# Performance work log

Hardware: AMD Instinct MI355X
Metric: run time of the kernel (lower is better)

## Reference

```python
import jax, jax.numpy as jnp
import numpy as np
import math

D_POLY = 2  # polynomial order d
N_NODES = 50000
IN_FEATS = 128
H_FEATS = 64
N_EDGES = 800000


def calc_thetas(d):
    # Beta-wavelet polynomial coefficients (ascending order), matching calculate_theta2
    thetas = []
    for i in range(d + 1):
        p = np.poly1d([1.0])
        for _ in range(i):
            p = p * np.poly1d([0.5, 0.0])      # (x/2)
        for _ in range(d - i):
            p = p * np.poly1d([-0.5, 1.0])     # (1 - x/2)
        beta = math.gamma(i + 1) * math.gamma(d + 1 - i) / math.gamma(d + 2)
        p = p / beta
        asc = p.coeffs[::-1]                   # ascending coefficients
        asc = np.concatenate([asc, np.zeros(d + 1 - len(asc))])
        thetas.append(asc.astype(np.float32))
    return thetas

THETAS = calc_thetas(D_POLY)


def setup_inputs() -> dict:
    key = jax.random.key(0)
    ks = jax.random.split(key, 7)
    features = jax.random.normal(ks[0], (N_NODES, IN_FEATS), dtype=jnp.float32)
    src = jax.random.randint(ks[1], (N_EDGES,), 0, N_NODES)
    dst = jax.random.randint(ks[2], (N_EDGES,), 0, N_NODES)
    s1 = 1.0 / math.sqrt(IN_FEATS)
    W1 = jax.random.uniform(ks[3], (H_FEATS, IN_FEATS), jnp.float32, -s1, s1)
    b1 = jnp.zeros((H_FEATS,), jnp.float32)
    s2 = 1.0 / math.sqrt(H_FEATS * (D_POLY + 1))
    W2 = jax.random.uniform(ks[4], (H_FEATS, H_FEATS * (D_POLY + 1)), jnp.float32, -s2, s2)
    b2 = jnp.zeros((H_FEATS,), jnp.float32)
    return {"features": features, "src": src, "dst": dst,
            "W1": W1, "b1": b1, "W2": W2, "b2": b2}


def reference(features, src, dst, W1, b1, W2, b2):
    N = features.shape[0]
    # linear1 + ReLU
    x = jax.nn.relu(features @ W1.T + b1)  # [N, H]
    # D^{-1/2} from in-degrees (clamped at 1)
    deg = jax.ops.segment_sum(jnp.ones_like(dst, dtype=x.dtype), dst, num_segments=N)
    D_invsqrt = jnp.clip(deg, 1.0, None) ** -0.5  # [N]
    D_invsqrt = D_invsqrt[:, None]

    def unn_laplacian(f):
        # f - D^{-1/2} A D^{-1/2} f   (aggregation onto destination nodes)
        agg = jax.ops.segment_sum((f * D_invsqrt)[src], dst, num_segments=N)
        return f - agg * D_invsqrt

    outs = []
    for theta in THETAS:
        f = x
        h = theta[0] * x
        for k in range(1, len(theta)):
            f = unn_laplacian(f)
            h = h + theta[k] * f
        outs.append(h)
    feats_final = jnp.concatenate(outs, axis=-1)  # [N, H*(d+1)]
    return feats_final @ W2.T + b2
```

## Files before the change

kernel.cpp:

```cpp
#include <hip/hip_runtime.h>

#define NN 50000
#define NE 800000
#define INF 128
#define HF 64
#define K2 192
#define MAXDEG 64

#if __has_builtin(__builtin_amdgcn_cvt_pk_fp8_f32) && __has_builtin(__builtin_amdgcn_cvt_pk_f32_fp8)
#define FP8_HW 1
#else
#include <hip/hip_fp8.h>
#endif

typedef __attribute__((ext_vector_type(8))) short short8;
typedef __attribute__((ext_vector_type(4))) float float4v;
typedef __attribute__((ext_vector_type(2))) float float2v;
typedef __attribute__((ext_vector_type(4))) unsigned short ushort4v;
typedef __attribute__((ext_vector_type(2))) unsigned int uint2v;

__device__ inline unsigned short f2bf(float x) {
    unsigned int u = __float_as_uint(x);
    u += 0x7FFFu + ((u >> 16) & 1u);
    return (unsigned short)(u >> 16);
}
__device__ inline float bflo(unsigned int p) { return __uint_as_float(p << 16); }
__device__ inline float bfhi(unsigned int p) { return __uint_as_float(p & 0xFFFF0000u); }


__device__ inline unsigned int fp8_pack4(float a, float b, float c, float d) {
#ifdef FP8_HW
    unsigned int w = (unsigned int)__builtin_amdgcn_cvt_pk_fp8_f32(a, b, 0, false);
    w = (unsigned int)__builtin_amdgcn_cvt_pk_fp8_f32(c, d, (int)w, true);
    return w;
#else
    __hip_fp8_e4m3 qa(a), qb(b), qc(c), qd(d);
    return (unsigned int)qa.__x | ((unsigned int)qb.__x << 8) |
           ((unsigned int)qc.__x << 16) | ((unsigned int)qd.__x << 24);
#endif
}
__device__ inline unsigned char fp8_1(float a) {
#ifdef FP8_HW
    return (unsigned char)((unsigned int)__builtin_amdgcn_cvt_pk_fp8_f32(a, 0.f, 0, false) & 0xFFu);
#else
    __hip_fp8_e4m3 q(a);
    return (unsigned char)q.__x;
#endif
}
__device__ inline float2v fp8_lo2(unsigned int d) {
#ifdef FP8_HW
    return __builtin_amdgcn_cvt_pk_f32_fp8((int)d, false);
#else
    __hip_fp8_e4m3 x; float2v r;
    x.__x = (unsigned char)(d & 0xFF);        r[0] = (float)x;
    x.__x = (unsigned char)((d >> 8) & 0xFF); r[1] = (float)x;
    return r;
#endif
}
__device__ inline float2v fp8_hi2(unsigned int d) {
#ifdef FP8_HW
    return __builtin_amdgcn_cvt_pk_f32_fp8((int)d, true);
#else
    __hip_fp8_e4m3 x; float2v r;
    x.__x = (unsigned char)((d >> 16) & 0xFF); r[0] = (float)x;
    x.__x = (unsigned char)((d >> 24) & 0xFF); r[1] = (float)x;
    return r;
#endif
}


__global__ __launch_bounds__(256) void fill_ell_part(const int* __restrict__ src,
                                                     const int* __restrict__ dst,
                                                     int* __restrict__ cnt,
                                                     unsigned short* __restrict__ ell) {
    int chunk = blockIdx.x >> 3;
    int p     = blockIdx.x & 7;
    int e0 = (chunk * 256 + (int)threadIdx.x) * 4;
    if (e0 >= NE) return;
    int4 d4 = *reinterpret_cast<const int4*>(dst + e0);
    int dd[4] = {d4.x, d4.y, d4.z, d4.w};
#pragma unroll
    for (int j = 0; j < 4; ++j) {
        int d = dd[j];
        if (d / 6250 == p) {
            int pos = atomicAdd(&cnt[d], 1);
            if (pos < MAXDEG) ell[d * MAXDEG + pos] = (unsigned short)src[e0 + j];
        }
    }
}


__global__ void pack_b(const float* __restrict__ W1, const float* __restrict__ W2,
                       unsigned short* __restrict__ Bp1, unsigned short* __restrict__ Bp2,
                       int* __restrict__ cnt,
                       unsigned int* __restrict__ hb0w, unsigned int* __restrict__ hb1w) {
    int gid = blockIdx.x * 256 + threadIdx.x;
    for (int z = gid; z < NN; z += 20480) cnt[z] = 0;
    if (gid < 16) {
        hb0w[(size_t)NN * 16 + gid] = 0;
        hb1w[(size_t)NN * 16 + gid] = 0;
    }
    if (gid >= 20480) return;
    if (gid < 8192) {
        int j  = gid & 7;
        int l  = (gid >> 3) & 63;
        int nt = (gid >> 9) & 3;
        int kc = gid >> 11;
        int n = nt * 16 + (l & 15);
        int k = kc * 32 + (l >> 4) * 8 + j;
        Bp1[gid] = f2bf(W1[n * INF + k]);
    } else {
        int g = gid - 8192;
        int j  = g & 7;
        int l  = (g >> 3) & 63;
        int nt = (g >> 9) & 3;
        int kc = g >> 11;
        int n = nt * 16 + (l & 15);
        int k = kc * 32 + (l >> 4) * 8 + j;
        const float* row = W2 + (size_t)n * K2;
        float v;
        if (k < 64) {
            v = 3.0f * row[k];
        } else if (k < 128) {
            int c = k - 64;
            v = -3.0f * row[c] + 3.0f * row[64 + c];
        } else {
            int c = k - 128;
            v = 0.75f * row[c] - 1.5f * row[64 + c] + 0.75f * row[128 + c];
        }
        Bp2[g] = f2bf(v);
    }
}


__global__ __launch_bounds__(256) void gemm1_mfma(const float* __restrict__ F,
                                                  const unsigned short* __restrict__ Bp,
                                                  const float* __restrict__ b1,
                                                  const int* __restrict__ cnt,
                                                  unsigned short* __restrict__ xb,
                                                  unsigned char* __restrict__ hb0) {
    int tid  = threadIdx.x;
    int lane = tid & 63;
    int wv   = tid >> 6;
    int m0   = blockIdx.x * 64 + wv * 16;
    if (m0 >= NN) return;
    int mrow = lane & 15;
    int q    = lane >> 4;

    float4v acc[4];
#pragma unroll
    for (int nt = 0; nt < 4; ++nt) acc[nt] = (float4v){0.f, 0.f, 0.f, 0.f};

    const float* arow = F + (size_t)(m0 + mrow) * INF + q * 8;
#pragma unroll
    for (int kc = 0; kc < INF / 32; ++kc) {
        const float* ap = arow + kc * 32;
        float4v a0 = *reinterpret_cast<const float4v*>(ap);
        float4v a1 = *reinterpret_cast<const float4v*>(ap + 4);
        short8 af;
        af[0] = (short)f2bf(a0[0]); af[1] = (short)f2bf(a0[1]);
        af[2] = (short)f2bf(a0[2]); af[3] = (short)f2bf(a0[3]);
        af[4] = (short)f2bf(a1[0]); af[5] = (short)f2bf(a1[1]);
        af[6] = (short)f2bf(a1[2]); af[7] = (short)f2bf(a1[3]);
#pragma unroll
        for (int nt = 0; nt < 4; ++nt) {
            short8 bf = *reinterpret_cast<const short8*>(Bp + (((kc * 4 + nt) * 64 + lane) << 3));
            acc[nt] = __builtin_amdgcn_mfma_f32_16x16x32_bf16(af, bf, acc[nt], 0, 0, 0);
        }
    }

    float dn[4];
#pragma unroll
    for (int r = 0; r < 4; ++r) {
        int c = cnt[m0 + q * 4 + r];
        c = c > MAXDEG ? MAXDEG : c;
        dn[r] = rsqrtf((float)(c < 1 ? 1 : c));
    }

#pragma unroll
    for (int nt = 0; nt < 4; ++nt) {
        int n = nt * 16 + mrow;
        float bv = b1[n];
#pragma unroll
        for (int r = 0; r < 4; ++r) {
            int node = m0 + q * 4 + r;
            float v = acc[nt][r] + bv;
            v = v > 0.0f ? v : 0.0f;
            xb [(size_t)node * HF + n] = f2bf(v);
            hb0[(size_t)node * HF + n] = fp8_1(v * dn[r]);
        }
    }
}


__device__ inline void gather_accum(const unsigned int* __restrict__ hbd,
                                    int s0, int s1, int s2, int s3,
                                    int deg, int base, int jj,
                                    float2v& e01, float2v& e23) {
    float2v A0 = {0.f, 0.f}, A1 = {0.f, 0.f};
    float2v B0 = {0.f, 0.f}, B1 = {0.f, 0.f};
    float2v C0 = {0.f, 0.f}, C1 = {0.f, 0.f};
    float2v D0 = {0.f, 0.f}, D1 = {0.f, 0.f};
    for (int k = 0; k < deg; k += 4) {
        int o = base + (k >> 2);
        int t0 = __shfl(s0, o), t1 = __shfl(s1, o);
        int t2 = __shfl(s2, o), t3 = __shfl(s3, o);
        unsigned int p0 = hbd[(size_t)t0 * 16 + jj];
        unsigned int p1 = hbd[(size_t)t1 * 16 + jj];
        unsigned int p2 = hbd[(size_t)t2 * 16 + jj];
        unsigned int p3 = hbd[(size_t)t3 * 16 + jj];
        A0 += fp8_lo2(p0); A1 += fp8_hi2(p0);
        B0 += fp8_lo2(p1); B1 += fp8_hi2(p1);
        C0 += fp8_lo2(p2); C1 += fp8_hi2(p2);
        D0 += fp8_lo2(p3); D1 += fp8_hi2(p3);
    }
    e01 = (A0 + B0) + (C0 + D0);
    e23 = (A1 + B1) + (C1 + D1);
}


__global__ __launch_bounds__(256) void gather_quad(const unsigned short* __restrict__ ell,
                                                   const int* __restrict__ cnt,
                                                   const unsigned short* __restrict__ fin,
                                                   const unsigned int* __restrict__ hb,
                                                   unsigned short* __restrict__ fout,
                                                   unsigned int* __restrict__ hout) {
    int lane  = threadIdx.x & 63;
    int wv    = threadIdx.x >> 6;
    int which = lane >> 4;
    int jj    = lane & 15;
    int n = blockIdx.x * 16 + wv * 4 + which;
    int deg = cnt[n];
    deg = deg > MAXDEG ? MAXDEG : deg;

    ushort4v ids = *reinterpret_cast<const ushort4v*>(ell + (size_t)n * MAXDEG + jj * 4);
    int slot = jj * 4;
    int s0 = (slot + 0 < deg) ? (int)ids[0] : NN;
    int s1 = (slot + 1 < deg) ? (int)ids[1] : NN;
    int s2 = (slot + 2 < deg) ? (int)ids[2] : NN;
    int s3 = (slot + 3 < deg) ? (int)ids[3] : NN;

    float2v e01, e23;
    gather_accum(hb, s0, s1, s2, s3, deg, which * 16, jj, e01, e23);

    float dn = rsqrtf((float)(deg < 1 ? 1 : deg));

    uint2v xv = ((const uint2v*)fin)[(size_t)n * 16 + jj];
    float f0 = bflo(xv[0]) - e01[0] * dn;
    float f1 = bfhi(xv[0]) - e01[1] * dn;
    float f2 = bflo(xv[1]) - e23[0] * dn;
    float f3 = bfhi(xv[1]) - e23[1] * dn;
    uint2v ov;
    ov[0] = (unsigned int)f2bf(f0) | ((unsigned int)f2bf(f1) << 16);
    ov[1] = (unsigned int)f2bf(f2) | ((unsigned int)f2bf(f3) << 16);
    ((uint2v*)fout)[(size_t)n * 16 + jj] = ov;
    hout[(size_t)n * 16 + jj] = fp8_pack4(f0 * dn, f1 * dn, f2 * dn, f3 * dn);
}


__global__ __launch_bounds__(256) void gather_gemm2(const unsigned short* __restrict__ ell,
                                                    const int* __restrict__ cnt,
                                                    const unsigned short* __restrict__ xb,
                                                    const unsigned short* __restrict__ f1b,
                                                    const unsigned int* __restrict__ hb1,
                                                    const unsigned short* __restrict__ Bp,
                                                    const float* __restrict__ b2,
                                                    float* __restrict__ out) {
    __shared__ __align__(16) unsigned int xl [16 * 68];
    __shared__ __align__(16) unsigned int f1l[16 * 68];
    __shared__ __align__(16) unsigned int f2l[16 * 68];
    int tid   = threadIdx.x;
    int lane  = tid & 63;
    int wv    = tid >> 6;
    int which = lane >> 4;
    int jj    = lane & 15;
    int row   = wv * 4 + which;
    int n     = blockIdx.x * 16 + row;

    int deg = cnt[n];
    deg = deg > MAXDEG ? MAXDEG : deg;
    ushort4v ids = *reinterpret_cast<const ushort4v*>(ell + (size_t)n * MAXDEG + jj * 4);
    int slot = jj * 4;
    int s0 = (slot + 0 < deg) ? (int)ids[0] : NN;
    int s1 = (slot + 1 < deg) ? (int)ids[1] : NN;
    int s2 = (slot + 2 < deg) ? (int)ids[2] : NN;
    int s3 = (slot + 3 < deg) ? (int)ids[3] : NN;

    float2v e01, e23;
    gather_accum(hb1, s0, s1, s2, s3, deg, which * 16, jj, e01, e23);

    float dn = rsqrtf((float)(deg < 1 ? 1 : deg));
    uint2v xv  = ((const uint2v*)f1b)[(size_t)n * 16 + jj];
    uint2v xbv = ((const uint2v*)xb )[(size_t)n * 16 + jj];
    float f0 = bflo(xv[0]) - e01[0] * dn;
    float f1 = bfhi(xv[0]) - e01[1] * dn;
    float f2 = bflo(xv[1]) - e23[0] * dn;
    float f3 = bfhi(xv[1]) - e23[1] * dn;

    int o = row * 68 + jj * 2;
    xl [o] = xbv[0]; xl [o + 1] = xbv[1];
    f1l[o] = xv[0];  f1l[o + 1] = xv[1];
    f2l[o]     = (unsigned int)f2bf(f0) | ((unsigned int)f2bf(f1) << 16);
    f2l[o + 1] = (unsigned int)f2bf(f2) | ((unsigned int)f2bf(f3) << 16);

    __syncthreads();

    int mrow = lane & 15;
    int qq   = lane >> 4;
    float4v acc = (float4v){0.f, 0.f, 0.f, 0.f};

#pragma unroll
    for (int kc = 0; kc < 6; ++kc) {
        const unsigned int* srcT = (kc < 2) ? xl : (kc < 4) ? f1l : f2l;
        int kk = kc & 1;
        short8 af = *reinterpret_cast<const short8*>(srcT + mrow * 68 + kk * 16 + qq * 4);
        short8 bf = *reinterpret_cast<const short8*>(Bp + (((kc * 4 + wv) * 64 + lane) << 3));
        acc = __builtin_amdgcn_mfma_f32_16x16x32_bf16(af, bf, acc, 0, 0, 0);
    }

    int n2 = wv * 16 + mrow;
    float bv = b2[n2];
    int nb = blockIdx.x * 16;
#pragma unroll
    for (int r = 0; r < 4; ++r) {
        int node = nb + qq * 4 + r;
        out[(size_t)node * HF + n2] = acc[r] + bv;
    }
}


extern "C" void kernel_launch(void* const* d_in, const int* in_sizes, int n_in,
                              void* d_out, int out_size, void* d_ws, size_t ws_size,
                              hipStream_t stream) {
    const float* features = (const float*)d_in[0];
    const int*   src      = (const int*)d_in[1];
    const int*   dst      = (const int*)d_in[2];
    const float* W1       = (const float*)d_in[3];
    const float* b1       = (const float*)d_in[4];
    const float* W2       = (const float*)d_in[5];
    const float* b2       = (const float*)d_in[6];
    float* out = (float*)d_out;

    unsigned short* xb  = (unsigned short*)d_ws;
    unsigned char*  hb0 = (unsigned char*)(xb + (size_t)NN * HF);
    unsigned short* f1b = (unsigned short*)(hb0 + (size_t)(NN + 1) * HF);
    unsigned char*  hb1 = (unsigned char*)(f1b + (size_t)NN * HF);
    unsigned short* Bp1 = (unsigned short*)(hb1 + (size_t)(NN + 1) * HF);
    unsigned short* Bp2 = Bp1 + 8192;
    unsigned short* ell = Bp2 + 12288;
    int*   cnt  = (int*)(ell + (size_t)NN * MAXDEG);

    pack_b<<<80, 256, 0, stream>>>(W1, W2, Bp1, Bp2, cnt,
                                   (unsigned int*)hb0, (unsigned int*)hb1);

    fill_ell_part<<<((NE + 1023) / 1024) * 8, 256, 0, stream>>>(src, dst, cnt, ell);

    gemm1_mfma<<<(NN + 63) / 64, 256, 0, stream>>>(features, Bp1, b1, cnt, xb, hb0);

    gather_quad<<<NN / 16, 256, 0, stream>>>(ell, cnt, xb, (const unsigned int*)hb0,
                                             f1b, (unsigned int*)hb1);

    gather_gemm2<<<NN / 16, 256, 0, stream>>>(ell, cnt, xb, f1b,
                                              (const unsigned int*)hb1, Bp2, b2, out);
}
```

Measured before the change: 158.5 us.

## Fuse all stages into one persistent kernel with grid-wide barriers

Replaces the five separate launches (weight packing, ELL fill, GEMM1, two gather stages) with a single persistent kernel of 1024 blocks. The blocks loop over virtual work items and synchronize between stages through an atomic-counter grid barrier. The counters and barrier word are zeroed with a memset before the launch. This removes per-launch overhead and inter-kernel gaps, but it depends on all 1024 blocks being co-resident, which launch_bounds(256,4) is meant to ensure. The barriers also serialize stages with spin-waiting, which can cost time when stages are unevenly loaded.

```diff
diff --git a/kernel.cpp b/kernel.cpp
--- a/kernel.cpp
+++ b/kernel.cpp
@@ -6,6 +6,10 @@
 #define HF 64
 #define K2 192
 #define MAXDEG 64
+#define GRID 1024
+#define ELLB (((NE + 1023) / 1024) * 8)
+#define G1B  ((NN + 63) / 64)
+#define GQB  (NN / 16)
 
 #if __has_builtin(__builtin_amdgcn_cvt_pk_fp8_f32) && __has_builtin(__builtin_amdgcn_cvt_pk_f32_fp8)
 #define FP8_HW 1
@@ -69,127 +73,14 @@
 }
 
 
-__global__ __launch_bounds__(256) void fill_ell_part(const int* __restrict__ src,
-                                                     const int* __restrict__ dst,
-                                                     int* __restrict__ cnt,
-                                                     unsigned short* __restrict__ ell) {
-    int chunk = blockIdx.x >> 3;
-    int p     = blockIdx.x & 7;
-    int e0 = (chunk * 256 + (int)threadIdx.x) * 4;
-    if (e0 >= NE) return;
-    int4 d4 = *reinterpret_cast<const int4*>(dst + e0);
-    int dd[4] = {d4.x, d4.y, d4.z, d4.w};
-#pragma unroll
-    for (int j = 0; j < 4; ++j) {
-        int d = dd[j];
-        if (d / 6250 == p) {
-            int pos = atomicAdd(&cnt[d], 1);
-            if (pos < MAXDEG) ell[d * MAXDEG + pos] = (unsigned short)src[e0 + j];
-        }
-    }
-}
-
-
-__global__ void pack_b(const float* __restrict__ W1, const float* __restrict__ W2,
-                       unsigned short* __restrict__ Bp1, unsigned short* __restrict__ Bp2,
-                       int* __restrict__ cnt,
-                       unsigned int* __restrict__ hb0w, unsigned int* __restrict__ hb1w) {
-    int gid = blockIdx.x * 256 + threadIdx.x;
-    for (int z = gid; z < NN; z += 20480) cnt[z] = 0;
-    if (gid < 16) {
-        hb0w[(size_t)NN * 16 + gid] = 0;
-        hb1w[(size_t)NN * 16 + gid] = 0;
-    }
-    if (gid >= 20480) return;
-    if (gid < 8192) {
-        int j  = gid & 7;
-        int l  = (gid >> 3) & 63;
-        int nt = (gid >> 9) & 3;
-        int kc = gid >> 11;
-        int n = nt * 16 + (l & 15);
-        int k = kc * 32 + (l >> 4) * 8 + j;
-        Bp1[gid] = f2bf(W1[n * INF + k]);
-    } else {
-        int g = gid - 8192;
-        int j  = g & 7;
-        int l  = (g >> 3) & 63;
-        int nt = (g >> 9) & 3;
-        int kc = g >> 11;
-        int n = nt * 16 + (l & 15);
-        int k = kc * 32 + (l >> 4) * 8 + j;
-        const float* row = W2 + (size_t)n * K2;
-        float v;
-        if (k < 64) {
-            v = 3.0f * row[k];
-        } else if (k < 128) {
-            int c = k - 64;
-            v = -3.0f * row[c] + 3.0f * row[64 + c];
-        } else {
-            int c = k - 128;
-            v = 0.75f * row[c] - 1.5f * row[64 + c] + 0.75f * row[128 + c];
-        }
-        Bp2[g] = f2bf(v);
-    }
-}
-
-
-__global__ __launch_bounds__(256) void gemm1_mfma(const float* __restrict__ F,
-                                                  const unsigned short* __restrict__ Bp,
-                                                  const float* __restrict__ b1,
-                                                  const int* __restrict__ cnt,
-                                                  unsigned short* __restrict__ xb,
-                                                  unsigned char* __restrict__ hb0) {
-    int tid  = threadIdx.x;
-    int lane = tid & 63;
-    int wv   = tid >> 6;
-    int m0   = blockIdx.x * 64 + wv * 16;
-    if (m0 >= NN) return;
-    int mrow = lane & 15;
-    int q    = lane >> 4;
-
-    float4v acc[4];
-#pragma unroll
-    for (int nt = 0; nt < 4; ++nt) acc[nt] = (float4v){0.f, 0.f, 0.f, 0.f};
-
-    const float* arow = F + (size_t)(m0 + mrow) * INF + q * 8;
-#pragma unroll
-    for (int kc = 0; kc < INF / 32; ++kc) {
-        const float* ap = arow + kc * 32;
-        float4v a0 = *reinterpret_cast<const float4v*>(ap);
-        float4v a1 = *reinterpret_cast<const float4v*>(ap + 4);
-        short8 af;
-        af[0] = (short)f2bf(a0[0]); af[1] = (short)f2bf(a0[1]);
-        af[2] = (short)f2bf(a0[2]); af[3] = (short)f2bf(a0[3]);
-        af[4] = (short)f2bf(a1[0]); af[5] = (short)f2bf(a1[1]);
-        af[6] = (short)f2bf(a1[2]); af[7] = (short)f2bf(a1[3]);
-#pragma unroll
-        for (int nt = 0; nt < 4; ++nt) {
-            short8 bf = *reinterpret_cast<const short8*>(Bp + (((kc * 4 + nt) * 64 + lane) << 3));
-            acc[nt] = __builtin_amdgcn_mfma_f32_16x16x32_bf16(af, bf, acc[nt], 0, 0, 0);
-        }
-    }
-
-    float dn[4];
-#pragma unroll
-    for (int r = 0; r < 4; ++r) {
-        int c = cnt[m0 + q * 4 + r];
-        c = c > MAXDEG ? MAXDEG : c;
-        dn[r] = rsqrtf((float)(c < 1 ? 1 : c));
-    }
-
-#pragma unroll
-    for (int nt = 0; nt < 4; ++nt) {
-        int n = nt * 16 + mrow;
-        float bv = b1[n];
-#pragma unroll
-        for (int r = 0; r < 4; ++r) {
-            int node = m0 + q * 4 + r;
-            float v = acc[nt][r] + bv;
-            v = v > 0.0f ? v : 0.0f;
-            xb [(size_t)node * HF + n] = f2bf(v);
-            hb0[(size_t)node * HF + n] = fp8_1(v * dn[r]);
-        }
-    }
+__device__ inline void gbar(unsigned int* bar, unsigned int target) {
+    __syncthreads();
+    if (threadIdx.x == 0) {
+        __hip_atomic_fetch_add(bar, 1u, __ATOMIC_ACQ_REL, __HIP_MEMORY_SCOPE_AGENT);
+        while (__hip_atomic_load(bar, __ATOMIC_ACQUIRE, __HIP_MEMORY_SCOPE_AGENT) < target)
+            __builtin_amdgcn_s_sleep(8);
+    }
+    __syncthreads();
 }
 
 
@@ -219,112 +110,217 @@
 }
 
 
-__global__ __launch_bounds__(256) void gather_quad(const unsigned short* __restrict__ ell,
-                                                   const int* __restrict__ cnt,
-                                                   const unsigned short* __restrict__ fin,
-                                                   const unsigned int* __restrict__ hb,
-                                                   unsigned short* __restrict__ fout,
-                                                   unsigned int* __restrict__ hout) {
-    int lane  = threadIdx.x & 63;
-    int wv    = threadIdx.x >> 6;
-    int which = lane >> 4;
-    int jj    = lane & 15;
-    int n = blockIdx.x * 16 + wv * 4 + which;
-    int deg = cnt[n];
-    deg = deg > MAXDEG ? MAXDEG : deg;
-
-    ushort4v ids = *reinterpret_cast<const ushort4v*>(ell + (size_t)n * MAXDEG + jj * 4);
-    int slot = jj * 4;
-    int s0 = (slot + 0 < deg) ? (int)ids[0] : NN;
-    int s1 = (slot + 1 < deg) ? (int)ids[1] : NN;
-    int s2 = (slot + 2 < deg) ? (int)ids[2] : NN;
-    int s3 = (slot + 3 < deg) ? (int)ids[3] : NN;
-
-    float2v e01, e23;
-    gather_accum(hb, s0, s1, s2, s3, deg, which * 16, jj, e01, e23);
-
-    float dn = rsqrtf((float)(deg < 1 ? 1 : deg));
-
-    uint2v xv = ((const uint2v*)fin)[(size_t)n * 16 + jj];
-    float f0 = bflo(xv[0]) - e01[0] * dn;
-    float f1 = bfhi(xv[0]) - e01[1] * dn;
-    float f2 = bflo(xv[1]) - e23[0] * dn;
-    float f3 = bfhi(xv[1]) - e23[1] * dn;
-    uint2v ov;
-    ov[0] = (unsigned int)f2bf(f0) | ((unsigned int)f2bf(f1) << 16);
-    ov[1] = (unsigned int)f2bf(f2) | ((unsigned int)f2bf(f3) << 16);
-    ((uint2v*)fout)[(size_t)n * 16 + jj] = ov;
-    hout[(size_t)n * 16 + jj] = fp8_pack4(f0 * dn, f1 * dn, f2 * dn, f3 * dn);
-}
-
-
-__global__ __launch_bounds__(256) void gather_gemm2(const unsigned short* __restrict__ ell,
-                                                    const int* __restrict__ cnt,
-                                                    const unsigned short* __restrict__ xb,
-                                                    const unsigned short* __restrict__ f1b,
-                                                    const unsigned int* __restrict__ hb1,
-                                                    const unsigned short* __restrict__ Bp,
-                                                    const float* __restrict__ b2,
-                                                    float* __restrict__ out) {
+__global__ __launch_bounds__(256, 4) void mega(
+        const float* __restrict__ F, const int* __restrict__ src,
+        const int* __restrict__ dst, const float* __restrict__ W1,
+        const float* __restrict__ b1, const float* __restrict__ W2,
+        const float* __restrict__ b2, float* __restrict__ out,
+        unsigned short* __restrict__ xb, unsigned char* __restrict__ hb0,
+        unsigned short* __restrict__ f1b, unsigned char* __restrict__ hb1,
+        unsigned short* __restrict__ Bp1, unsigned short* __restrict__ Bp2,
+        unsigned short* __restrict__ ell, int* __restrict__ cnt,
+        unsigned int* __restrict__ bar) {
     __shared__ __align__(16) unsigned int xl [16 * 68];
     __shared__ __align__(16) unsigned int f1l[16 * 68];
     __shared__ __align__(16) unsigned int f2l[16 * 68];
+
     int tid   = threadIdx.x;
     int lane  = tid & 63;
     int wv    = tid >> 6;
     int which = lane >> 4;
     int jj    = lane & 15;
-    int row   = wv * 4 + which;
-    int n     = blockIdx.x * 16 + row;
-
-    int deg = cnt[n];
-    deg = deg > MAXDEG ? MAXDEG : deg;
-    ushort4v ids = *reinterpret_cast<const ushort4v*>(ell + (size_t)n * MAXDEG + jj * 4);
-    int slot = jj * 4;
-    int s0 = (slot + 0 < deg) ? (int)ids[0] : NN;
-    int s1 = (slot + 1 < deg) ? (int)ids[1] : NN;
-    int s2 = (slot + 2 < deg) ? (int)ids[2] : NN;
-    int s3 = (slot + 3 < deg) ? (int)ids[3] : NN;
-
-    float2v e01, e23;
-    gather_accum(hb1, s0, s1, s2, s3, deg, which * 16, jj, e01, e23);
-
-    float dn = rsqrtf((float)(deg < 1 ? 1 : deg));
-    uint2v xv  = ((const uint2v*)f1b)[(size_t)n * 16 + jj];
-    uint2v xbv = ((const uint2v*)xb )[(size_t)n * 16 + jj];
-    float f0 = bflo(xv[0]) - e01[0] * dn;
-    float f1 = bfhi(xv[0]) - e01[1] * dn;
-    float f2 = bflo(xv[1]) - e23[0] * dn;
-    float f3 = bfhi(xv[1]) - e23[1] * dn;
-
-    int o = row * 68 + jj * 2;
-    xl [o] = xbv[0]; xl [o + 1] = xbv[1];
-    f1l[o] = xv[0];  f1l[o + 1] = xv[1];
-    f2l[o]     = (unsigned int)f2bf(f0) | ((unsigned int)f2bf(f1) << 16);
-    f2l[o + 1] = (unsigned int)f2bf(f2) | ((unsigned int)f2bf(f3) << 16);
-
-    __syncthreads();
-
-    int mrow = lane & 15;
-    int qq   = lane >> 4;
-    float4v acc = (float4v){0.f, 0.f, 0.f, 0.f};
-
-#pragma unroll
-    for (int kc = 0; kc < 6; ++kc) {
-        const unsigned int* srcT = (kc < 2) ? xl : (kc < 4) ? f1l : f2l;
-        int kk = kc & 1;
-        short8 af = *reinterpret_cast<const short8*>(srcT + mrow * 68 + kk * 16 + qq * 4);
-        short8 bf = *reinterpret_cast<const short8*>(Bp + (((kc * 4 + wv) * 64 + lane) << 3));
-        acc = __builtin_amdgcn_mfma_f32_16x16x32_bf16(af, bf, acc, 0, 0, 0);
-    }
-
-    int n2 = wv * 16 + mrow;
-    float bv = b2[n2];
-    int nb = blockIdx.x * 16;
-#pragma unroll
-    for (int r = 0; r < 4; ++r) {
-        int node = nb + qq * 4 + r;
-        out[(size_t)node * HF + n2] = acc[r] + bv;
+
+    {
+        int gid = blockIdx.x * 256 + tid;
+        if (gid < 16) {
+            ((unsigned int*)hb0)[(size_t)NN * 16 + gid] = 0;
+            ((unsigned int*)hb1)[(size_t)NN * 16 + gid] = 0;
+        }
+        if (gid < 8192) {
+            int j  = gid & 7;
+            int l  = (gid >> 3) & 63;
+            int nt = (gid >> 9) & 3;
+            int kc = gid >> 11;
+            int n = nt * 16 + (l & 15);
+            int k = kc * 32 + (l >> 4) * 8 + j;
+            Bp1[gid] = f2bf(W1[n * INF + k]);
+        } else if (gid < 20480) {
+            int g = gid - 8192;
+            int j  = g & 7;
+            int l  = (g >> 3) & 63;
+            int nt = (g >> 9) & 3;
+            int kc = g >> 11;
+            int n = nt * 16 + (l & 15);
+            int k = kc * 32 + (l >> 4) * 8 + j;
+            const float* row = W2 + (size_t)n * K2;
+            float v;
+            if (k < 64) {
+                v = 3.0f * row[k];
+            } else if (k < 128) {
+                int c = k - 64;
+                v = -3.0f * row[c] + 3.0f * row[64 + c];
+            } else {
+                int c = k - 128;
+                v = 0.75f * row[c] - 1.5f * row[64 + c] + 0.75f * row[128 + c];
+            }
+            Bp2[g] = f2bf(v);
+        }
+    }
+
+    for (int vb = blockIdx.x; vb < ELLB; vb += GRID) {
+        int chunk = vb >> 3;
+        int p     = vb & 7;
+        int e0 = (chunk * 256 + tid) * 4;
+        if (e0 >= NE) continue;
+        int4 d4 = *reinterpret_cast<const int4*>(dst + e0);
+        int dd[4] = {d4.x, d4.y, d4.z, d4.w};
+#pragma unroll
+        for (int j = 0; j < 4; ++j) {
+            int d = dd[j];
+            if (d / 6250 == p) {
+                int pos = atomicAdd(&cnt[d], 1);
+                if (pos < MAXDEG) ell[d * MAXDEG + pos] = (unsigned short)src[e0 + j];
+            }
+        }
+    }
+    gbar(bar, GRID);
+
+    for (int tb = blockIdx.x; tb < G1B; tb += GRID) {
+        int m0 = tb * 64 + wv * 16;
+        if (m0 >= NN) continue;
+        int mrow = lane & 15;
+        int q    = lane >> 4;
+
+        float4v acc[4];
+#pragma unroll
+        for (int nt = 0; nt < 4; ++nt) acc[nt] = (float4v){0.f, 0.f, 0.f, 0.f};
+
+        const float* arow = F + (size_t)(m0 + mrow) * INF + q * 8;
+#pragma unroll
+        for (int kc = 0; kc < INF / 32; ++kc) {
+            const float* ap = arow + kc * 32;
+            float4v a0 = *reinterpret_cast<const float4v*>(ap);
+            float4v a1 = *reinterpret_cast<const float4v*>(ap + 4);
+            short8 af;
+            af[0] = (short)f2bf(a0[0]); af[1] = (short)f2bf(a0[1]);
+            af[2] = (short)f2bf(a0[2]); af[3] = (short)f2bf(a0[3]);
+            af[4] = (short)f2bf(a1[0]); af[5] = (short)f2bf(a1[1]);
+            af[6] = (short)f2bf(a1[2]); af[7] = (short)f2bf(a1[3]);
+#pragma unroll
+            for (int nt = 0; nt < 4; ++nt) {
+                short8 bf = *reinterpret_cast<const short8*>(Bp1 + (((kc * 4 + nt) * 64 + lane) << 3));
+                acc[nt] = __builtin_amdgcn_mfma_f32_16x16x32_bf16(af, bf, acc[nt], 0, 0, 0);
+            }
+        }
+
+        float dn[4];
+#pragma unroll
+        for (int r = 0; r < 4; ++r) {
+            int c = cnt[m0 + q * 4 + r];
+            c = c > MAXDEG ? MAXDEG : c;
+            dn[r] = rsqrtf((float)(c < 1 ? 1 : c));
+        }
+
+#pragma unroll
+        for (int nt = 0; nt < 4; ++nt) {
+            int n = nt * 16 + mrow;
+            float bv = b1[n];
+#pragma unroll
+            for (int r = 0; r < 4; ++r) {
+                int node = m0 + q * 4 + r;
+                float v = acc[nt][r] + bv;
+                v = v > 0.0f ? v : 0.0f;
+                xb [(size_t)node * HF + n] = f2bf(v);
+                hb0[(size_t)node * HF + n] = fp8_1(v * dn[r]);
+            }
+        }
+    }
+    gbar(bar, 2 * GRID);
+
+    for (int vb = blockIdx.x; vb < GQB; vb += GRID) {
+        int n = vb * 16 + wv * 4 + which;
+        int deg = cnt[n];
+        deg = deg > MAXDEG ? MAXDEG : deg;
+
+        ushort4v ids = *reinterpret_cast<const ushort4v*>(ell + (size_t)n * MAXDEG + jj * 4);
+        int slot = jj * 4;
+        int s0 = (slot + 0 < deg) ? (int)ids[0] : NN;
+        int s1 = (slot + 1 < deg) ? (int)ids[1] : NN;
+        int s2 = (slot + 2 < deg) ? (int)ids[2] : NN;
+        int s3 = (slot + 3 < deg) ? (int)ids[3] : NN;
+
+        float2v e01, e23;
+        gather_accum((const unsigned int*)hb0, s0, s1, s2, s3, deg, which * 16, jj, e01, e23);
+
+        float dn = rsqrtf((float)(deg < 1 ? 1 : deg));
+
+        uint2v xv = ((const uint2v*)xb)[(size_t)n * 16 + jj];
+        float f0 = bflo(xv[0]) - e01[0] * dn;
+        float f1 = bfhi(xv[0]) - e01[1] * dn;
+        float f2 = bflo(xv[1]) - e23[0] * dn;
+        float f3 = bfhi(xv[1]) - e23[1] * dn;
+        uint2v ov;
+        ov[0] = (unsigned int)f2bf(f0) | ((unsigned int)f2bf(f1) << 16);
+        ov[1] = (unsigned int)f2bf(f2) | ((unsigned int)f2bf(f3) << 16);
+        ((uint2v*)f1b)[(size_t)n * 16 + jj] = ov;
+        ((unsigned int*)hb1)[(size_t)n * 16 + jj] = fp8_pack4(f0 * dn, f1 * dn, f2 * dn, f3 * dn);
+    }
+    gbar(bar, 3 * GRID);
+
+    for (int vb = blockIdx.x; vb < GQB; vb += GRID) {
+        int row = wv * 4 + which;
+        int n   = vb * 16 + row;
+
+        int deg = cnt[n];
+        deg = deg > MAXDEG ? MAXDEG : deg;
+        ushort4v ids = *reinterpret_cast<const ushort4v*>(ell + (size_t)n * MAXDEG + jj * 4);
+        int slot = jj * 4;
+        int s0 = (slot + 0 < deg) ? (int)ids[0] : NN;
+        int s1 = (slot + 1 < deg) ? (int)ids[1] : NN;
+        int s2 = (slot + 2 < deg) ? (int)ids[2] : NN;
+        int s3 = (slot + 3 < deg) ? (int)ids[3] : NN;
+
+        float2v e01, e23;
+        gather_accum((const unsigned int*)hb1, s0, s1, s2, s3, deg, which * 16, jj, e01, e23);
+
+        float dn = rsqrtf((float)(deg < 1 ? 1 : deg));
+        uint2v xv  = ((const uint2v*)f1b)[(size_t)n * 16 + jj];
+        uint2v xbv = ((const uint2v*)xb )[(size_t)n * 16 + jj];
+        float f0 = bflo(xv[0]) - e01[0] * dn;
+        float f1 = bfhi(xv[0]) - e01[1] * dn;
+        float f2 = bflo(xv[1]) - e23[0] * dn;
+        float f3 = bfhi(xv[1]) - e23[1] * dn;
+
+        int o = row * 68 + jj * 2;
+        xl [o] = xbv[0]; xl [o + 1] = xbv[1];
+        f1l[o] = xv[0];  f1l[o + 1] = xv[1];
+        f2l[o]     = (unsigned int)f2bf(f0) | ((unsigned int)f2bf(f1) << 16);
+        f2l[o + 1] = (unsigned int)f2bf(f2) | ((unsigned int)f2bf(f3) << 16);
+
+        __syncthreads();
+
+        int mrow = lane & 15;
+        int qq   = lane >> 4;
+        float4v acc = (float4v){0.f, 0.f, 0.f, 0.f};
+
+#pragma unroll
+        for (int kc = 0; kc < 6; ++kc) {
+            const unsigned int* srcT = (kc < 2) ? xl : (kc < 4) ? f1l : f2l;
+            int kk = kc & 1;
+            short8 af = *reinterpret_cast<const short8*>(srcT + mrow * 68 + kk * 16 + qq * 4);
+            short8 bf = *reinterpret_cast<const short8*>(Bp2 + (((kc * 4 + wv) * 64 + lane) << 3));
+            acc = __builtin_amdgcn_mfma_f32_16x16x32_bf16(af, bf, acc, 0, 0, 0);
+        }
+
+        int n2 = wv * 16 + mrow;
+        float bv = b2[n2];
+        int nb = vb * 16;
+#pragma unroll
+        for (int r = 0; r < 4; ++r) {
+            int node = nb + qq * 4 + r;
+            out[(size_t)node * HF + n2] = acc[r] + bv;
+        }
+        __syncthreads();
     }
 }
 
@@ -349,17 +345,10 @@
     unsigned short* Bp2 = Bp1 + 8192;
     unsigned short* ell = Bp2 + 12288;
     int*   cnt  = (int*)(ell + (size_t)NN * MAXDEG);
-
-    pack_b<<<80, 256, 0, stream>>>(W1, W2, Bp1, Bp2, cnt,
-                                   (unsigned int*)hb0, (unsigned int*)hb1);
-
-    fill_ell_part<<<((NE + 1023) / 1024) * 8, 256, 0, stream>>>(src, dst, cnt, ell);
-
-    gemm1_mfma<<<(NN + 63) / 64, 256, 0, stream>>>(features, Bp1, b1, cnt, xb, hb0);
-
-    gather_quad<<<NN / 16, 256, 0, stream>>>(ell, cnt, xb, (const unsigned int*)hb0,
-                                             f1b, (unsigned int*)hb1);
-
-    gather_gemm2<<<NN / 16, 256, 0, stream>>>(ell, cnt, xb, f1b,
-                                              (const unsigned int*)hb1, Bp2, b2, out);
-}
+    unsigned int* bar = (unsigned int*)(cnt + NN);
+
+    hipMemsetAsync(cnt, 0, (size_t)NN * 4 + 64, stream);
+
+    mega<<<GRID, 256, 0, stream>>>(features, src, dst, W1, b1, W2, b2, out,
+                                   xb, hb0, f1b, hb1, Bp1, Bp2, ell, cnt, bar);
+}
```

Measured after the change: 538.0 us. +239.5%, slower.
